# Performance work log

Hardware: AMD Instinct MI355X
Metric: run time of the kernel (lower is better)

## Reference

```python
import jax, jax.numpy as jnp
import numpy as np

B, NG, GS, H = 256, 3008, 10, 6          # batch, n_genes, genes per leaf term, hidden per term
T = [2048, 256, 32, 1]                    # terms per DAG level (leaves -> root)
IN = [GS, 8 * H, 8 * H, 32 * H]           # per-term input size at each level
EPS = 1e-5


def setup_inputs() -> dict:
    keys = iter(jax.random.split(jax.random.key(0), 64))

    def rn(shape, s=0.1):
        return jax.random.normal(next(keys), shape, dtype=jnp.float32) * s

    d = {"x": rn((B, NG), 1.0),
         "gW": rn((T[0], GS, NG)),   # stacked leaf direct_gene_layer weights
         "gb": rn((T[0], GS))}
    for l in range(4):
        t, i = T[l], IN[l]
        d[f"w{l}"] = rn((t, H, i))          # term linear weight
        d[f"b{l}"] = rn((t, H))             # term linear bias
        d[f"g{l}"] = jnp.ones((t, H), jnp.float32)   # BN gamma
        d[f"e{l}"] = jnp.zeros((t, H), jnp.float32)  # BN beta
        d[f"p{l}"] = rn((t, H))             # aux linear1 weight (H->1)
        d[f"q{l}"] = rn((t,))               # aux linear1 bias
        d[f"r{l}"] = rn((t,))               # aux linear2 weight (1->1)
        d[f"s{l}"] = rn((t,))               # aux linear2 bias
    d["fw"] = rn((2 * H, H)); d["fb"] = rn((2 * H,))
    d["fg"] = jnp.ones((2 * H,), jnp.float32); d["fe"] = jnp.zeros((2 * H,), jnp.float32)
    d["pw"] = rn((1, 2 * H)); d["pb"] = rn((1,))
    d["rw"] = rn((1, 1)); d["rb"] = rn((1,))
    return d


def _bn(z, g, b):
    # BatchNorm1d in training mode: biased batch stats over axis 0
    m = z.mean(0)
    v = ((z - m) ** 2).mean(0)
    return (z - m) * jax.lax.rsqrt(v + EPS) * g + b


def reference(x, gW, gb,
              w0, b0, g0, e0, p0, q0, r0, s0,
              w1, b1, g1, e1, p1, q1, r1, s1,
              w2, b2, g2, e2, p2, q2, r2, s2,
              w3, b3, g3, e3, p3, q3, r3, s3,
              fw, fb, fg, fe, pw, pb, rw, rb):
    Bn = x.shape[0]
    # stacked direct gene layers for all leaf terms: [B, T0, GS]
    h = jnp.einsum('bn,tgn->btg', x, gW) + gb
    levels = [(w0, b0, g0, e0, p0, q0, r0, s0),
              (w1, b1, g1, e1, p1, q1, r1, s1),
              (w2, b2, g2, e2, p2, q2, r2, s2),
              (w3, b3, g3, e3, p3, q3, r3, s3)]
    aux = []
    for (w, b, g, e, p, q, r, s) in levels:
        # children of term t are contiguous -> concat == reshape
        hin = h.reshape(Bn, w.shape[0], w.shape[2])      # [B, T_l, in_l]
        z = jnp.tanh(jnp.einsum('bti,thi->bth', hin, w) + b)
        y = _bn(z, g, e)                                  # term_NN_out_map
        aux.append(r * jnp.tanh(jnp.einsum('bth,th->bt', y, p) + q) + s)
        h = y
    yroot = h.reshape(Bn, H)                              # root output [B, H]
    of = _bn(jnp.tanh(yroot @ fw.T + fb), fg, fe)         # final BN [B, 2H]
    auxf = jnp.tanh(of @ pw.T + pb) @ rw.T + rb           # final aux [B, 1]
    return jnp.concatenate(aux + [auxf], axis=1)          # [B, 2048+256+32+1+1]
```

## Files before the change

kernel.cpp:

```cpp
#include <hip/hip_runtime.h>
#include <hip/hip_bf16.h>
#include <stdint.h>

#define EPS 1e-5f
#define NOUT 2338

typedef __bf16 bf16x8 __attribute__((ext_vector_type(8)));
typedef float f32x4 __attribute__((ext_vector_type(4)));
typedef unsigned short u16;

__device__ __forceinline__ uint32_t pack2f(float lo, float hi) {
  union { __bf16 h[2]; uint32_t u; } r;
  r.h[0] = (__bf16)lo;
  r.h[1] = (__bf16)hi;
  return r.u;
}

__global__ __launch_bounds__(256) void cvt_pack_kernel(const float* __restrict__ x,
                                                       u16* __restrict__ xbp) {
  const int i = blockIdx.x * 256 + threadIdx.x;
  const int ks = i >> 10;
  const int rem = i & 1023;
  const int kb = rem >> 8;
  const int m = rem & 255;
  const f32x4* src = (const f32x4*)(x + (size_t)m * 3008 + ks * 32 + kb * 8);
  f32x4 a = src[0], b = src[1];
  uint4 o;
  o.x = pack2f(a.x, a.y);
  o.y = pack2f(a.z, a.w);
  o.z = pack2f(b.x, b.y);
  o.w = pack2f(b.z, b.w);
  ((uint4*)xbp)[i] = o;
}

__global__ __launch_bounds__(256, 3) void gemm_leaf(const float* __restrict__ W,
                                                    const float* __restrict__ gb,
                                                    const u16* __restrict__ XBp,
                                                    float* __restrict__ hout) {
  __shared__ __align__(16) u16 xl[2][8192];
  __shared__ __align__(16) float wlds[2][2048];
  const int tid = threadIdx.x;
  const int w = tid >> 6;
  const int lane = tid & 63;
  const int rh = w >> 1;
  const int mh = w & 1;
  const int lquad = lane >> 4;
  const int lmod = lane & 15;
  const int n0 = (blockIdx.x >> 1) * 64;
  const int kh = blockIdx.x & 1;
  const int kbase = kh * 47;

  f32x4 acc[2][8];
#pragma unroll
  for (int a = 0; a < 2; ++a)
#pragma unroll
    for (int j = 0; j < 8; ++j) acc[a][j] = (f32x4){0.f, 0.f, 0.f, 0.f};

#define STAGE_X(ks, buf)                                                                \
  {                                                                                     \
    _Pragma("unroll")                                                                   \
    for (int p = 0; p < 4; ++p) {                                                       \
      const int c = (w * 4 + p) * 64;                                                   \
      const u16* src = XBp + (size_t)(ks) * 8192 + (size_t)(c + lane) * 8;              \
      u16* dst = &xl[buf][(size_t)c * 8];                                               \
      __builtin_amdgcn_global_load_lds((const __attribute__((address_space(1))) void*)src, \
                                       (__attribute__((address_space(3))) void*)dst,    \
                                       16, 0, 0);                                       \
    }                                                                                   \
  }

  const int wr0 = w * 2, wr1 = w * 2 + 1;
  const int lrow = lane >> 3;
  const int lswf = ((((lane & 7) * 16) ^ (lrow << 4)) >> 2);
  const float* wsrc0 = W + (size_t)(n0 + wr0 * 8 + lrow) * 3008 + lswf;
  const float* wsrc1 = W + (size_t)(n0 + wr1 * 8 + lrow) * 3008 + lswf;
#define STAGE_W(ks, buf)                                                                \
  {                                                                                     \
    __builtin_amdgcn_global_load_lds(                                                   \
        (const __attribute__((address_space(1))) void*)(wsrc0 + (size_t)(ks) * 32),     \
        (__attribute__((address_space(3))) void*)&wlds[buf][wr0 * 256], 16, 0, 0);      \
    __builtin_amdgcn_global_load_lds(                                                   \
        (const __attribute__((address_space(1))) void*)(wsrc1 + (size_t)(ks) * 32),     \
        (__attribute__((address_space(3))) void*)&wlds[buf][wr1 * 256], 16, 0, 0);      \
  }

  STAGE_X(kbase, 0);
  STAGE_W(kbase, 0);

  const int xorv = (lmod & 7) << 4;
  for (int s = 0; s < 47; ++s) {
    const int buf = s & 1;
    __syncthreads();
    if (s < 46) {
      STAGE_X(kbase + s + 1, buf ^ 1);
      STAGE_W(kbase + s + 1, buf ^ 1);
    }
    __builtin_amdgcn_sched_barrier(0);

    const float* wbase = &wlds[buf][0];
    const u16* xb = &xl[buf][(size_t)lquad * 2048 + mh * 1024 + lmod * 8];
    union { uint32_t u32[4]; bf16x8 v; } af[2];
#pragma unroll
    for (int a = 0; a < 2; ++a) {
      const int row = rh * 32 + a * 16 + lmod;
      const int fb = row * 32;
      const f32x4 wlo = *(const f32x4*)(wbase + fb + (((lquad * 32) ^ xorv) >> 2));
      const f32x4 whi = *(const f32x4*)(wbase + fb + (((lquad * 32 + 16) ^ xorv) >> 2));
      af[a].u32[0] = pack2f(wlo.x, wlo.y);
      af[a].u32[1] = pack2f(wlo.z, wlo.w);
      af[a].u32[2] = pack2f(whi.x, whi.y);
      af[a].u32[3] = pack2f(whi.z, whi.w);
    }
#pragma unroll
    for (int j = 0; j < 8; ++j) {
      const bf16x8 bfrag = *(const bf16x8*)(xb + j * 128);
      acc[0][j] = __builtin_amdgcn_mfma_f32_16x16x32_bf16(af[0].v, bfrag, acc[0][j], 0, 0, 0);
      acc[1][j] = __builtin_amdgcn_mfma_f32_16x16x32_bf16(af[1].v, bfrag, acc[1][j], 0, 0, 0);
    }
  }

#undef STAGE_W
#undef STAGE_X

  float* hp = hout + (size_t)kh * 20480 * 256;
#pragma unroll
  for (int a = 0; a < 2; ++a) {
    const int r0 = n0 + rh * 32 + a * 16 + lquad * 4;
    float gb4[4];
#pragma unroll
    for (int r2 = 0; r2 < 4; ++r2) gb4[r2] = (kh == 0) ? gb[r0 + r2] : 0.f;
#pragma unroll
    for (int j = 0; j < 8; ++j) {
      const int col = (mh * 8 + j) * 16 + lmod;
#pragma unroll
      for (int r2 = 0; r2 < 4; ++r2) {
        hp[(size_t)(r0 + r2) * 256 + col] = acc[a][j][r2] + gb4[r2];
      }
    }
  }
}

__global__ __launch_bounds__(256) void level0_kernel(
    const float* __restrict__ yinA, const float* __restrict__ yinB,
    const float* __restrict__ w,
    const float* __restrict__ bia, const float* __restrict__ gam,
    const float* __restrict__ bet, const float* __restrict__ p,
    const float* __restrict__ q, const float* __restrict__ r,
    const float* __restrict__ s, float* __restrict__ yout,
    float* __restrict__ out, int inl, int off) {
  const int t = blockIdx.x;
  const int b = threadIdx.x;
  __shared__ float wls[6 * 10];
  __shared__ float part[4][12];
  __shared__ float stats[12];
  const float* wt = w + (size_t)t * 6 * inl;
  for (int i = b; i < 6 * inl; i += 256) wls[i] = wt[i];
  __syncthreads();

  float z[6];
#pragma unroll
  for (int h = 0; h < 6; ++h) z[h] = bia[t * 6 + h];
  const float* ypA = yinA + (size_t)t * inl * 256 + b;
  const float* ypB = yinB + (size_t)t * inl * 256 + b;
  for (int i = 0; i < inl; ++i) {
    float v = ypA[(size_t)i * 256] + ypB[(size_t)i * 256];
#pragma unroll
    for (int h = 0; h < 6; ++h) z[h] = fmaf(v, wls[h * inl + i], z[h]);
  }
#pragma unroll
  for (int h = 0; h < 6; ++h) z[h] = tanhf(z[h]);

  float sm[6], sq[6];
#pragma unroll
  for (int h = 0; h < 6; ++h) { sm[h] = z[h]; sq[h] = z[h] * z[h]; }
#pragma unroll
  for (int o = 32; o > 0; o >>= 1) {
#pragma unroll
    for (int h = 0; h < 6; ++h) {
      sm[h] += __shfl_down(sm[h], o);
      sq[h] += __shfl_down(sq[h], o);
    }
  }
  const int lane = b & 63, wvi = b >> 6;
  if (lane == 0) {
#pragma unroll
    for (int h = 0; h < 6; ++h) { part[wvi][h] = sm[h]; part[wvi][6 + h] = sq[h]; }
  }
  __syncthreads();
  if (b < 6) {
    float msum = part[0][b] + part[1][b] + part[2][b] + part[3][b];
    float qsum = part[0][6 + b] + part[1][6 + b] + part[2][6 + b] + part[3][6 + b];
    float m = msum * (1.f / 256.f);
    float var = qsum * (1.f / 256.f) - m * m;
    stats[b] = m;
    stats[6 + b] = rsqrtf(var + EPS);
  }
  __syncthreads();

  float a = q[t];
#pragma unroll
  for (int h = 0; h < 6; ++h) {
    float yy = (z[h] - stats[h]) * stats[6 + h] * gam[t * 6 + h] + bet[t * 6 + h];
    yout[((size_t)t * 6 + h) * 256 + b] = yy;
    a = fmaf(yy, p[t * 6 + h], a);
  }
  out[(size_t)b * NOUT + off + t] = tanhf(a) * r[t] + s[t];
}

__global__ __launch_bounds__(256) void level_kernel(
    const float* __restrict__ yin, const float* __restrict__ w,
    const float* __restrict__ bia, const float* __restrict__ gam,
    const float* __restrict__ bet, const float* __restrict__ p,
    const float* __restrict__ q, const float* __restrict__ r,
    const float* __restrict__ s, float* __restrict__ yout,
    float* __restrict__ out, int inl, int off) {
  const int t = blockIdx.x;
  const int b = threadIdx.x;
  __shared__ float wls[6 * 48];
  __shared__ float part[4][12];
  __shared__ float stats[12];
  const float* wt = w + (size_t)t * 6 * inl;
  for (int i = b; i < 6 * inl; i += 256) wls[i] = wt[i];
  __syncthreads();

  float z[6];
#pragma unroll
  for (int h = 0; h < 6; ++h) z[h] = bia[t * 6 + h];
  const float* yp = yin + (size_t)t * inl * 256 + b;
  for (int i = 0; i < inl; ++i) {
    float v = yp[(size_t)i * 256];
#pragma unroll
    for (int h = 0; h < 6; ++h) z[h] = fmaf(v, wls[h * inl + i], z[h]);
  }
#pragma unroll
  for (int h = 0; h < 6; ++h) z[h] = tanhf(z[h]);

  float sm[6], sq[6];
#pragma unroll
  for (int h = 0; h < 6; ++h) { sm[h] = z[h]; sq[h] = z[h] * z[h]; }
#pragma unroll
  for (int o = 32; o > 0; o >>= 1) {
#pragma unroll
    for (int h = 0; h < 6; ++h) {
      sm[h] += __shfl_down(sm[h], o);
      sq[h] += __shfl_down(sq[h], o);
    }
  }
  const int lane = b & 63, wvi = b >> 6;
  if (lane == 0) {
#pragma unroll
    for (int h = 0; h < 6; ++h) { part[wvi][h] = sm[h]; part[wvi][6 + h] = sq[h]; }
  }
  __syncthreads();
  if (b < 6) {
    float msum = part[0][b] + part[1][b] + part[2][b] + part[3][b];
    float qsum = part[0][6 + b] + part[1][6 + b] + part[2][6 + b] + part[3][6 + b];
    float m = msum * (1.f / 256.f);
    float var = qsum * (1.f / 256.f) - m * m;
    stats[b] = m;
    stats[6 + b] = rsqrtf(var + EPS);
  }
  __syncthreads();

  float a = q[t];
#pragma unroll
  for (int h = 0; h < 6; ++h) {
    float yy = (z[h] - stats[h]) * stats[6 + h] * gam[t * 6 + h] + bet[t * 6 + h];
    yout[((size_t)t * 6 + h) * 256 + b] = yy;
    a = fmaf(yy, p[t * 6 + h], a);
  }
  out[(size_t)b * NOUT + off + t] = tanhf(a) * r[t] + s[t];
}

__global__ __launch_bounds__(256) void level3_final_kernel(
    const float* __restrict__ y2,
    const float* __restrict__ w3, const float* __restrict__ b3,
    const float* __restrict__ g3, const float* __restrict__ e3,
    const float* __restrict__ p3, const float* __restrict__ q3,
    const float* __restrict__ r3, const float* __restrict__ s3,
    const float* __restrict__ fw, const float* __restrict__ fb,
    const float* __restrict__ fg, const float* __restrict__ fe,
    const float* __restrict__ pw, const float* __restrict__ pb,
    const float* __restrict__ rw, const float* __restrict__ rb,
    float* __restrict__ out) {
  const int b = threadIdx.x;
  __shared__ float wls[6 * 192];
  __shared__ float part[4][24];
  __shared__ float stats[24];
  for (int i = b; i < 6 * 192; i += 256) wls[i] = w3[i];
  __syncthreads();

  float z[6];
#pragma unroll
  for (int h = 0; h < 6; ++h) z[h] = b3[h];
  const float* yp = y2 + b;
  for (int i = 0; i < 192; ++i) {
    float v = yp[(size_t)i * 256];
#pragma unroll
    for (int h = 0; h < 6; ++h) z[h] = fmaf(v, wls[h * 192 + i], z[h]);
  }
#pragma unroll
  for (int h = 0; h < 6; ++h) z[h] = tanhf(z[h]);

  const int lane = b & 63, wvi = b >> 6;
  {
    float sm[6], sq[6];
#pragma unroll
    for (int h = 0; h < 6; ++h) { sm[h] = z[h]; sq[h] = z[h] * z[h]; }
#pragma unroll
    for (int o = 32; o > 0; o >>= 1) {
#pragma unroll
      for (int h = 0; h < 6; ++h) {
        sm[h] += __shfl_down(sm[h], o);
        sq[h] += __shfl_down(sq[h], o);
      }
    }
    if (lane == 0) {
#pragma unroll
      for (int h = 0; h < 6; ++h) { part[wvi][h] = sm[h]; part[wvi][6 + h] = sq[h]; }
    }
    __syncthreads();
    if (b < 6) {
      float msum = part[0][b] + part[1][b] + part[2][b] + part[3][b];
      float qsum = part[0][6 + b] + part[1][6 + b] + part[2][6 + b] + part[3][6 + b];
      float m = msum * (1.f / 256.f);
      float var = qsum * (1.f / 256.f) - m * m;
      stats[b] = m;
      stats[6 + b] = rsqrtf(var + EPS);
    }
    __syncthreads();
  }

  float yr[6];
  float a3 = q3[0];
#pragma unroll
  for (int h = 0; h < 6; ++h) {
    yr[h] = (z[h] - stats[h]) * stats[6 + h] * g3[h] + e3[h];
    a3 = fmaf(yr[h], p3[h], a3);
  }
  out[(size_t)b * NOUT + 2336] = tanhf(a3) * r3[0] + s3[0];
  __syncthreads();

  float zf[12];
#pragma unroll
  for (int j = 0; j < 12; ++j) {
    float a = fb[j];
#pragma unroll
    for (int h = 0; h < 6; ++h) a = fmaf(yr[h], fw[j * 6 + h], a);
    zf[j] = tanhf(a);
  }
  {
    float sm[12], sq[12];
#pragma unroll
    for (int j = 0; j < 12; ++j) { sm[j] = zf[j]; sq[j] = zf[j] * zf[j]; }
#pragma unroll
    for (int o = 32; o > 0; o >>= 1) {
#pragma unroll
      for (int j = 0; j < 12; ++j) {
        sm[j] += __shfl_down(sm[j], o);
        sq[j] += __shfl_down(sq[j], o);
      }
    }
    if (lane == 0) {
#pragma unroll
      for (int j = 0; j < 12; ++j) { part[wvi][j] = sm[j]; part[wvi][12 + j] = sq[j]; }
    }
    __syncthreads();
    if (b < 12) {
      float msum = part[0][b] + part[1][b] + part[2][b] + part[3][b];
      float qsum = part[0][12 + b] + part[1][12 + b] + part[2][12 + b] + part[3][12 + b];
      float m = msum * (1.f / 256.f);
      float var = qsum * (1.f / 256.f) - m * m;
      stats[b] = m;
      stats[12 + b] = rsqrtf(var + EPS);
    }
    __syncthreads();
  }
  float a = pb[0];
#pragma unroll
  for (int j = 0; j < 12; ++j) {
    float of = (zf[j] - stats[j]) * stats[12 + j] * fg[j] + fe[j];
    a = fmaf(of, pw[j], a);
  }
  out[(size_t)b * NOUT + 2337] = tanhf(a) * rw[0] + rb[0];
}

extern "C" void kernel_launch(void* const* d_in, const int* in_sizes, int n_in,
                              void* d_out, int out_size, void* d_ws, size_t ws_size,
                              hipStream_t stream) {
  const float* x  = (const float*)d_in[0];
  const float* gW = (const float*)d_in[1];
  const float* gb = (const float*)d_in[2];
  float* out = (float*)d_out;

  char* wsb = (char*)d_ws;
  u16* XBp = (u16*)wsb;
  float* h0 = (float*)(wsb + 1540096);
  float* y0 = h0 + (size_t)2 * 20480 * 256;
  float* y1 = y0 + (size_t)12288 * 256;
  float* y2 = y1 + (size_t)1536 * 256;

  cvt_pack_kernel<<<dim3(376), dim3(256), 0, stream>>>(x, XBp);
  gemm_leaf<<<dim3(640), dim3(256), 0, stream>>>(gW, gb, XBp, h0);

  level0_kernel<<<dim3(2048), dim3(256), 0, stream>>>(
      h0, h0 + (size_t)20480 * 256,
      (const float*)d_in[3], (const float*)d_in[4], (const float*)d_in[5],
      (const float*)d_in[6], (const float*)d_in[7], (const float*)d_in[8],
      (const float*)d_in[9], (const float*)d_in[10], y0, out, 10, 0);

#define LV(base, yin, yout, inl, off, grid)                                           \
  level_kernel<<<dim3(grid), dim3(256), 0, stream>>>(                                 \
      yin, (const float*)d_in[base], (const float*)d_in[base + 1],                    \
      (const float*)d_in[base + 2], (const float*)d_in[base + 3],                     \
      (const float*)d_in[base + 4], (const float*)d_in[base + 5],                     \
      (const float*)d_in[base + 6], (const float*)d_in[base + 7], yout, out, inl, off)

  LV(11, y0, y1, 48,  2048, 256);
  LV(19, y1, y2, 48,  2304, 32);
#undef LV

  level3_final_kernel<<<dim3(1), dim3(256), 0, stream>>>(
      y2,
      (const float*)d_in[27], (const float*)d_in[28], (const float*)d_in[29],
      (const float*)d_in[30], (const float*)d_in[31], (const float*)d_in[32],
      (const float*)d_in[33], (const float*)d_in[34],
      (const float*)d_in[35], (const float*)d_in[36], (const float*)d_in[37],
      (const float*)d_in[38], (const float*)d_in[39], (const float*)d_in[40],
      (const float*)d_in[41], (const float*)d_in[42], out);
}
```

Before: 137.1 us.

## Load X fragments directly to registers and give each wave private W tiles

The activation pack kernel now writes X in MFMA fragment order, so each wave loads its B fragments straight from global memory into registers, double-buffered in two register sets. The X LDS staging is gone. Each wave also stages only its own 32 weight rows into a private LDS slice, which lets the block-wide __syncthreads be replaced by explicit vmcnt waits. The intent is to remove block barriers and LDS traffic for X from the main loop. In exchange it raises register use (occupancy hint drops from 3 to 2 blocks per CU) and each wave pair now re-reads the same X fragments from global/L2.

```diff
diff --git a/kernel.cpp b/kernel.cpp
--- a/kernel.cpp
+++ b/kernel.cpp
@@ -17,28 +17,33 @@
 }
 
 __global__ __launch_bounds__(256) void cvt_pack_kernel(const float* __restrict__ x,
-                                                       u16* __restrict__ xbp) {
+                                                       u16* __restrict__ xb2) {
   const int i = blockIdx.x * 256 + threadIdx.x;
-  const int ks = i >> 10;
-  const int rem = i & 1023;
-  const int kb = rem >> 8;
-  const int m = rem & 255;
-  const f32x4* src = (const f32x4*)(x + (size_t)m * 3008 + ks * 32 + kb * 8);
+  const int c = i >> 6;
+  const int l = i & 63;
+  const int ks = c >> 4;
+  const int rem = c & 15;
+  const int mh = rem >> 3;
+  const int j = rem & 7;
+  const int lquad = l >> 4;
+  const int lmod = l & 15;
+  const int m = mh * 128 + j * 16 + lmod;
+  const int k0 = ks * 32 + lquad * 8;
+  const f32x4* src = (const f32x4*)(x + (size_t)m * 3008 + k0);
   f32x4 a = src[0], b = src[1];
   uint4 o;
   o.x = pack2f(a.x, a.y);
   o.y = pack2f(a.z, a.w);
   o.z = pack2f(b.x, b.y);
   o.w = pack2f(b.z, b.w);
-  ((uint4*)xbp)[i] = o;
-}
-
-__global__ __launch_bounds__(256, 3) void gemm_leaf(const float* __restrict__ W,
+  ((uint4*)xb2)[i] = o;
+}
+
+__global__ __launch_bounds__(256, 2) void gemm_leaf(const float* __restrict__ W,
                                                     const float* __restrict__ gb,
-                                                    const u16* __restrict__ XBp,
+                                                    const u16* __restrict__ XB2,
                                                     float* __restrict__ hout) {
-  __shared__ __align__(16) u16 xl[2][8192];
-  __shared__ __align__(16) float wlds[2][2048];
+  __shared__ __align__(16) float wsl[2][4][1024];
   const int tid = threadIdx.x;
   const int w = tid >> 6;
   const int lane = tid & 63;
@@ -56,71 +61,80 @@
 #pragma unroll
     for (int j = 0; j < 8; ++j) acc[a][j] = (f32x4){0.f, 0.f, 0.f, 0.f};
 
-#define STAGE_X(ks, buf)                                                                \
-  {                                                                                     \
+  const int lrow = lane >> 3;
+  const int lswf = ((((lane & 7) * 16) ^ (lrow << 4)) >> 2);
+  const float* wsrc[4];
+#pragma unroll
+  for (int q = 0; q < 4; ++q)
+    wsrc[q] = W + (size_t)(n0 + rh * 32 + q * 8 + lrow) * 3008 + lswf;
+
+#define STAGE_W(t, buf)                                                                 \
+  do {                                                                                  \
     _Pragma("unroll")                                                                   \
-    for (int p = 0; p < 4; ++p) {                                                       \
-      const int c = (w * 4 + p) * 64;                                                   \
-      const u16* src = XBp + (size_t)(ks) * 8192 + (size_t)(c + lane) * 8;              \
-      u16* dst = &xl[buf][(size_t)c * 8];                                               \
+    for (int q = 0; q < 4; ++q) {                                                       \
+      const float* src = wsrc[q] + (size_t)(t) * 32;                                    \
+      float* dst = &wsl[buf][w][q * 256];                                               \
       __builtin_amdgcn_global_load_lds((const __attribute__((address_space(1))) void*)src, \
                                        (__attribute__((address_space(3))) void*)dst,    \
                                        16, 0, 0);                                       \
     }                                                                                   \
-  }
-
-  const int wr0 = w * 2, wr1 = w * 2 + 1;
-  const int lrow = lane >> 3;
-  const int lswf = ((((lane & 7) * 16) ^ (lrow << 4)) >> 2);
-  const float* wsrc0 = W + (size_t)(n0 + wr0 * 8 + lrow) * 3008 + lswf;
-  const float* wsrc1 = W + (size_t)(n0 + wr1 * 8 + lrow) * 3008 + lswf;
-#define STAGE_W(ks, buf)                                                                \
-  {                                                                                     \
-    __builtin_amdgcn_global_load_lds(                                                   \
-        (const __attribute__((address_space(1))) void*)(wsrc0 + (size_t)(ks) * 32),     \
-        (__attribute__((address_space(3))) void*)&wlds[buf][wr0 * 256], 16, 0, 0);      \
-    __builtin_amdgcn_global_load_lds(                                                   \
-        (const __attribute__((address_space(1))) void*)(wsrc1 + (size_t)(ks) * 32),     \
-        (__attribute__((address_space(3))) void*)&wlds[buf][wr1 * 256], 16, 0, 0);      \
-  }
-
-  STAGE_X(kbase, 0);
+  } while (0)
+
+  const u16* xbase = XB2 + (size_t)mh * 8 * 512 + lane * 8;
+#define LOADX(t, DST)                                                                   \
+  do {                                                                                  \
+    const u16* xp = xbase + (size_t)(t) * 16 * 512;                                     \
+    _Pragma("unroll")                                                                   \
+    for (int j = 0; j < 8; ++j) DST[j] = *(const bf16x8*)(xp + j * 512);                \
+  } while (0)
+
+  const int xorv = (lmod & 7) << 4;
+
+#define BODY(s, CUR, NXT, VMX, ISSUE)                                                   \
+  do {                                                                                  \
+    asm volatile("s_waitcnt vmcnt(8)" ::: "memory");                   \
+    __builtin_amdgcn_sched_barrier(0);                                                  \
+    if (ISSUE) STAGE_W(kbase + (s) + 1, ((s) + 1) & 1);                                 \
+    __builtin_amdgcn_sched_barrier(0);                                                  \
+    if (ISSUE) LOADX(kbase + (s) + 1, NXT);                                             \
+    __builtin_amdgcn_sched_barrier(0);                                                  \
+    asm volatile("s_waitcnt vmcnt(" #VMX ")" ::: "memory");           \
+    __builtin_amdgcn_sched_barrier(0);                                                  \
+    const float* fb = &wsl[(s) & 1][w][0];                                              \
+    union { uint32_t u32[4]; bf16x8 v; } af[2];                                         \
+    _Pragma("unroll")                                                                   \
+    for (int a = 0; a < 2; ++a) {                                                       \
+      const float* rowp = fb + (a * 16 + lmod) * 32;                                    \
+      const f32x4 wlo = *(const f32x4*)(rowp + (((lquad * 32) ^ xorv) >> 2));           \
+      const f32x4 whi = *(const f32x4*)(rowp + (((lquad * 32 + 16) ^ xorv) >> 2));      \
+      af[a].u32[0] = pack2f(wlo.x, wlo.y);                                              \
+      af[a].u32[1] = pack2f(wlo.z, wlo.w);                                              \
+      af[a].u32[2] = pack2f(whi.x, whi.y);                                              \
+      af[a].u32[3] = pack2f(whi.z, whi.w);                                              \
+    }                                                                                   \
+    _Pragma("unroll")                                                                   \
+    for (int j = 0; j < 8; ++j) {                                                       \
+      acc[0][j] = __builtin_amdgcn_mfma_f32_16x16x32_bf16(af[0].v, CUR[j], acc[0][j], 0, 0, 0); \
+      acc[1][j] = __builtin_amdgcn_mfma_f32_16x16x32_bf16(af[1].v, CUR[j], acc[1][j], 0, 0, 0); \
+    }                                                                                   \
+  } while (0)
+
+  bf16x8 B0[8], B1[8];
   STAGE_W(kbase, 0);
-
-  const int xorv = (lmod & 7) << 4;
-  for (int s = 0; s < 47; ++s) {
-    const int buf = s & 1;
-    __syncthreads();
-    if (s < 46) {
-      STAGE_X(kbase + s + 1, buf ^ 1);
-      STAGE_W(kbase + s + 1, buf ^ 1);
-    }
-    __builtin_amdgcn_sched_barrier(0);
-
-    const float* wbase = &wlds[buf][0];
-    const u16* xb = &xl[buf][(size_t)lquad * 2048 + mh * 1024 + lmod * 8];
-    union { uint32_t u32[4]; bf16x8 v; } af[2];
-#pragma unroll
-    for (int a = 0; a < 2; ++a) {
-      const int row = rh * 32 + a * 16 + lmod;
-      const int fb = row * 32;
-      const f32x4 wlo = *(const f32x4*)(wbase + fb + (((lquad * 32) ^ xorv) >> 2));
-      const f32x4 whi = *(const f32x4*)(wbase + fb + (((lquad * 32 + 16) ^ xorv) >> 2));
-      af[a].u32[0] = pack2f(wlo.x, wlo.y);
-      af[a].u32[1] = pack2f(wlo.z, wlo.w);
-      af[a].u32[2] = pack2f(whi.x, whi.y);
-      af[a].u32[3] = pack2f(whi.z, whi.w);
-    }
-#pragma unroll
-    for (int j = 0; j < 8; ++j) {
-      const bf16x8 bfrag = *(const bf16x8*)(xb + j * 128);
-      acc[0][j] = __builtin_amdgcn_mfma_f32_16x16x32_bf16(af[0].v, bfrag, acc[0][j], 0, 0, 0);
-      acc[1][j] = __builtin_amdgcn_mfma_f32_16x16x32_bf16(af[1].v, bfrag, acc[1][j], 0, 0, 0);
-    }
-  }
-
+  __builtin_amdgcn_sched_barrier(0);
+  LOADX(kbase, B0);
+  __builtin_amdgcn_sched_barrier(0);
+
+  for (int ss = 0; ss < 23; ++ss) {
+    const int s = ss * 2;
+    BODY(s, B0, B1, 12, true);
+    BODY(s + 1, B1, B0, 12, true);
+  }
+  BODY(46, B0, B1, 0, false);
+
+#undef BODY
+#undef LOADX
 #undef STAGE_W
-#undef STAGE_X
 
   float* hp = hout + (size_t)kh * 20480 * 256;
 #pragma unroll
@@ -394,14 +408,14 @@
   float* out = (float*)d_out;
 
   char* wsb = (char*)d_ws;
-  u16* XBp = (u16*)wsb;
+  u16* XB2 = (u16*)wsb;
   float* h0 = (float*)(wsb + 1540096);
   float* y0 = h0 + (size_t)2 * 20480 * 256;
   float* y1 = y0 + (size_t)12288 * 256;
   float* y2 = y1 + (size_t)1536 * 256;
 
-  cvt_pack_kernel<<<dim3(376), dim3(256), 0, stream>>>(x, XBp);
-  gemm_leaf<<<dim3(640), dim3(256), 0, stream>>>(gW, gb, XBp, h0);
+  cvt_pack_kernel<<<dim3(376), dim3(256), 0, stream>>>(x, XB2);
+  gemm_leaf<<<dim3(640), dim3(256), 0, stream>>>(gW, gb, XB2, h0);
 
   level0_kernel<<<dim3(2048), dim3(256), 0, stream>>>(
       h0, h0 + (size_t)20480 * 256,
```

After: 172.3 us. 1.26x slower.

## Triple-buffer leaf GEMM LDS stages with explicit vmcnt waits

Applied to the files above, without the earlier changes.

Moves the leaf GEMM from double to triple buffering of the X and W tiles in LDS, prefetching two K-steps ahead. A partial s_waitcnt vmcnt(6) replaces the full wait at each barrier, so the next stage's global-to-LDS loads can stay in flight during compute. The larger LDS footprint lowers the occupancy target from 3 to 2 blocks per CU. The vmcnt count and the final tail-buffer index have to match the loop exactly, or reads will race.

```diff
diff --git a/kernel.cpp b/kernel.cpp
--- a/kernel.cpp
+++ b/kernel.cpp
@@ -33,12 +33,12 @@
   ((uint4*)xbp)[i] = o;
 }
 
-__global__ __launch_bounds__(256, 3) void gemm_leaf(const float* __restrict__ W,
+__global__ __launch_bounds__(256, 2) void gemm_leaf(const float* __restrict__ W,
                                                     const float* __restrict__ gb,
                                                     const u16* __restrict__ XBp,
                                                     float* __restrict__ hout) {
-  __shared__ __align__(16) u16 xl[2][8192];
-  __shared__ __align__(16) float wlds[2][2048];
+  __shared__ __align__(16) u16 xl[3][8192];
+  __shared__ __align__(16) float wlds[3][2048];
   const int tid = threadIdx.x;
   const int w = tid >> 6;
   const int lane = tid & 63;
@@ -56,8 +56,14 @@
 #pragma unroll
     for (int j = 0; j < 8; ++j) acc[a][j] = (f32x4){0.f, 0.f, 0.f, 0.f};
 
-#define STAGE_X(ks, buf)                                                                \
-  {                                                                                     \
+  const int wr0 = w * 2, wr1 = w * 2 + 1;
+  const int lrow = lane >> 3;
+  const int lswf = ((((lane & 7) * 16) ^ (lrow << 4)) >> 2);
+  const float* wsrc0 = W + (size_t)(n0 + wr0 * 8 + lrow) * 3008 + lswf;
+  const float* wsrc1 = W + (size_t)(n0 + wr1 * 8 + lrow) * 3008 + lswf;
+
+#define STAGE(ks, buf)                                                                  \
+  do {                                                                                  \
     _Pragma("unroll")                                                                   \
     for (int p = 0; p < 4; ++p) {                                                       \
       const int c = (w * 4 + p) * 64;                                                   \
@@ -67,60 +73,64 @@
                                        (__attribute__((address_space(3))) void*)dst,    \
                                        16, 0, 0);                                       \
     }                                                                                   \
-  }
-
-  const int wr0 = w * 2, wr1 = w * 2 + 1;
-  const int lrow = lane >> 3;
-  const int lswf = ((((lane & 7) * 16) ^ (lrow << 4)) >> 2);
-  const float* wsrc0 = W + (size_t)(n0 + wr0 * 8 + lrow) * 3008 + lswf;
-  const float* wsrc1 = W + (size_t)(n0 + wr1 * 8 + lrow) * 3008 + lswf;
-#define STAGE_W(ks, buf)                                                                \
-  {                                                                                     \
     __builtin_amdgcn_global_load_lds(                                                   \
         (const __attribute__((address_space(1))) void*)(wsrc0 + (size_t)(ks) * 32),     \
         (__attribute__((address_space(3))) void*)&wlds[buf][wr0 * 256], 16, 0, 0);      \
     __builtin_amdgcn_global_load_lds(                                                   \
         (const __attribute__((address_space(1))) void*)(wsrc1 + (size_t)(ks) * 32),     \
         (__attribute__((address_space(3))) void*)&wlds[buf][wr1 * 256], 16, 0, 0);      \
-  }
-
-  STAGE_X(kbase, 0);
-  STAGE_W(kbase, 0);
+  } while (0)
 
   const int xorv = (lmod & 7) << 4;
-  for (int s = 0; s < 47; ++s) {
-    const int buf = s & 1;
-    __syncthreads();
-    if (s < 46) {
-      STAGE_X(kbase + s + 1, buf ^ 1);
-      STAGE_W(kbase + s + 1, buf ^ 1);
-    }
+
+#define COMPUTE(buf)                                                                    \
+  do {                                                                                  \
+    const float* wbase = &wlds[buf][0];                                                 \
+    const u16* xb = &xl[buf][(size_t)lquad * 2048 + mh * 1024 + lmod * 8];              \
+    union { uint32_t u32[4]; bf16x8 v; } af[2];                                         \
+    _Pragma("unroll")                                                                   \
+    for (int a = 0; a < 2; ++a) {                                                       \
+      const int row = rh * 32 + a * 16 + lmod;                                          \
+      const float* rowp = wbase + row * 32;                                             \
+      const f32x4 wlo = *(const f32x4*)(rowp + (((lquad * 32) ^ xorv) >> 2));           \
+      const f32x4 whi = *(const f32x4*)(rowp + (((lquad * 32 + 16) ^ xorv) >> 2));      \
+      af[a].u32[0] = pack2f(wlo.x, wlo.y);                                              \
+      af[a].u32[1] = pack2f(wlo.z, wlo.w);                                              \
+      af[a].u32[2] = pack2f(whi.x, whi.y);                                              \
+      af[a].u32[3] = pack2f(whi.z, whi.w);                                              \
+    }                                                                                   \
+    _Pragma("unroll")                                                                   \
+    for (int j = 0; j < 8; ++j) {                                                       \
+      const bf16x8 bfrag = *(const bf16x8*)(xb + j * 128);                              \
+      acc[0][j] = __builtin_amdgcn_mfma_f32_16x16x32_bf16(af[0].v, bfrag, acc[0][j], 0, 0, 0); \
+      acc[1][j] = __builtin_amdgcn_mfma_f32_16x16x32_bf16(af[1].v, bfrag, acc[1][j], 0, 0, 0); \
+    }                                                                                   \
+  } while (0)
+
+  STAGE(kbase + 0, 0);
+  __builtin_amdgcn_sched_barrier(0);
+  STAGE(kbase + 1, 1);
+  __builtin_amdgcn_sched_barrier(0);
+
+  for (int s = 0; s < 46; ++s) {
+    asm volatile("s_waitcnt vmcnt(6)" ::: "memory");
     __builtin_amdgcn_sched_barrier(0);
-
-    const float* wbase = &wlds[buf][0];
-    const u16* xb = &xl[buf][(size_t)lquad * 2048 + mh * 1024 + lmod * 8];
-    union { uint32_t u32[4]; bf16x8 v; } af[2];
-#pragma unroll
-    for (int a = 0; a < 2; ++a) {
-      const int row = rh * 32 + a * 16 + lmod;
-      const int fb = row * 32;
-      const f32x4 wlo = *(const f32x4*)(wbase + fb + (((lquad * 32) ^ xorv) >> 2));
-      const f32x4 whi = *(const f32x4*)(wbase + fb + (((lquad * 32 + 16) ^ xorv) >> 2));
-      af[a].u32[0] = pack2f(wlo.x, wlo.y);
-      af[a].u32[1] = pack2f(wlo.z, wlo.w);
-      af[a].u32[2] = pack2f(whi.x, whi.y);
-      af[a].u32[3] = pack2f(whi.z, whi.w);
-    }
-#pragma unroll
-    for (int j = 0; j < 8; ++j) {
-      const bf16x8 bfrag = *(const bf16x8*)(xb + j * 128);
-      acc[0][j] = __builtin_amdgcn_mfma_f32_16x16x32_bf16(af[0].v, bfrag, acc[0][j], 0, 0, 0);
-      acc[1][j] = __builtin_amdgcn_mfma_f32_16x16x32_bf16(af[1].v, bfrag, acc[1][j], 0, 0, 0);
-    }
-  }
-
-#undef STAGE_W
-#undef STAGE_X
+    __builtin_amdgcn_s_barrier();
+    __builtin_amdgcn_sched_barrier(0);
+    if (s + 2 <= 46) {
+      STAGE(kbase + s + 2, (s + 2) % 3);
+    }
+    __builtin_amdgcn_sched_barrier(0);
+    COMPUTE(s % 3);
+  }
+  asm volatile("s_waitcnt vmcnt(0)" ::: "memory");
+  __builtin_amdgcn_sched_barrier(0);
+  __builtin_amdgcn_s_barrier();
+  __builtin_amdgcn_sched_barrier(0);
+  COMPUTE(1);
+
+#undef COMPUTE
+#undef STAGE
 
   float* hp = hout + (size_t)kh * 20480 * 256;
 #pragma unroll
```

Measured after the change: 175.0 us. +27.7%, slower.
